# Optimization experiments

Measured on AMD Instinct MI355X. Metric: run time of the kernel, lower is better.

## Reference

```python
import jax, jax.numpy as jnp
import numpy as np

N = 32768   # total nodes
B = 128     # graphs
S = 256     # nodes per graph (equal-size graphs)
E = 524288  # edges
DIN = 128   # in_dim
DH = 256    # hidden_dim
H = 8       # heads
DFF = 1024  # ffn hidden
EPS = 1e-5


def _seg_sum(x, idx, num):
    return jax.ops.segment_sum(x, idx, num_segments=num)


def _bn(x, g, b):
    # BatchNorm1d with batch statistics (training-mode math, deterministic)
    mu = jnp.mean(x, axis=0)
    var = jnp.mean((x - mu) ** 2, axis=0)
    return (x - mu) * jax.lax.rsqrt(var + EPS) * g + b


def _ln(x, g, b):
    mu = jnp.mean(x, axis=-1, keepdims=True)
    var = jnp.mean((x - mu) ** 2, axis=-1, keepdims=True)
    return (x - mu) * jax.lax.rsqrt(var + EPS) * g + b


def _gcn_conv(x, W, bias, edge_index, n):
    # PyG GCNConv: h = x W; add self-loops; norm = d^-1/2[row] * d^-1/2[col]; scatter-add at col
    h = x @ W
    loop = jnp.arange(n)
    row = jnp.concatenate([edge_index[0], loop])
    col = jnp.concatenate([edge_index[1], loop])
    deg = _seg_sum(jnp.ones_like(col, dtype=h.dtype), col, n)  # >=1 due to self-loops
    dis = jax.lax.rsqrt(jnp.maximum(deg, 1.0))
    norm = dis[row] * dis[col]
    out = _seg_sum(h[row] * norm[:, None], col, n)
    return out + bias


def setup_inputs() -> dict:
    key = jax.random.key(0)
    ks = jax.random.split(key, 24)

    def w(i, shape, scale=0.05):
        return jax.random.normal(ks[i], shape, dtype=jnp.float32) * scale

    return {
        "x": jax.random.normal(ks[0], (N, DIN), dtype=jnp.float32),
        "edge_index": jax.random.randint(ks[1], (2, E), 0, N, dtype=jnp.int32),
        "batch": jnp.repeat(jnp.arange(B, dtype=jnp.int32), S),
        "inter_f": jax.random.normal(ks[2], (B, DH), dtype=jnp.float32),
        "bn1_g": jnp.ones((DIN,), jnp.float32), "bn1_b": jnp.zeros((DIN,), jnp.float32),
        "bn2_g": jnp.ones((DH,), jnp.float32), "bn2_b": jnp.zeros((DH,), jnp.float32),
        "w_conv1": w(3, (DIN, DH)), "b_conv1": jnp.zeros((DH,), jnp.float32),
        "w_conv2": w(4, (DH, DH)), "b_conv2": jnp.zeros((DH,), jnp.float32),
        "wq": w(5, (DH, DH)), "bq": jnp.zeros((DH,), jnp.float32),
        "wk": w(6, (DH, DH)), "bk": jnp.zeros((DH,), jnp.float32),
        "wv": w(7, (DH, DH)), "bv": jnp.zeros((DH,), jnp.float32),
        "wo": w(8, (DH, DH)), "bo": jnp.zeros((DH,), jnp.float32),
        "ln1_g": jnp.ones((DH,), jnp.float32), "ln1_b": jnp.zeros((DH,), jnp.float32),
        "ln2_g": jnp.ones((DH,), jnp.float32), "ln2_b": jnp.zeros((DH,), jnp.float32),
        "w_ff1": w(9, (DH, DFF)), "b_ff1": jnp.zeros((DFF,), jnp.float32),
        "w_ff2": w(10, (DFF, DH)), "b_ff2": jnp.zeros((DH,), jnp.float32),
    }


def reference(x, edge_index, batch, inter_f,
              bn1_g, bn1_b, bn2_g, bn2_b,
              w_conv1, b_conv1, w_conv2, b_conv2,
              wq, bq, wk, bk, wv, bv, wo, bo,
              ln1_g, ln1_b, ln2_g, ln2_b,
              w_ff1, b_ff1, w_ff2, b_ff2):
    n = x.shape[0]
    hd = DH // H
    # init_avg_h: scatter-mean of raw x per graph
    cnt = _seg_sum(jnp.ones((n,), x.dtype), batch, B)
    init_avg_h = _seg_sum(x, batch, B) / jnp.maximum(cnt, 1.0)[:, None]
    # layer 1 (dropout = identity in eval)
    h = _bn(x, bn1_g, bn1_b)
    h = jax.nn.relu(_gcn_conv(h, w_conv1, b_conv1, edge_index, n))
    # layer 2 with residual
    pre = h
    h2 = _bn(h, bn2_g, bn2_b)
    h = pre + jax.nn.relu(_gcn_conv(h2, w_conv2, b_conv2, edge_index, n))
    # transformer block: inject per-graph feature, self-attend within each graph
    inter_h = inter_f[batch]
    t = (h + inter_h).reshape(B, S, DH)
    q = (t @ wq + bq).reshape(B, S, H, hd)
    k = (t @ wk + bk).reshape(B, S, H, hd)
    v = (t @ wv + bv).reshape(B, S, H, hd)
    scores = jnp.einsum('bqhd,bkhd->bhqk', q, k) / jnp.sqrt(jnp.float32(hd))
    attn = jax.nn.softmax(scores, axis=-1)
    o = jnp.einsum('bhqk,bkhd->bqhd', attn, v).reshape(B, S, DH) @ wo + bo
    t2 = _ln(t + o, ln1_g, ln1_b)
    ffn = jax.nn.relu(t2 @ w_ff1 + b_ff1) @ w_ff2 + b_ff2
    t3 = _ln(t2 + ffn, ln2_g, ln2_b)
    hg = t3.reshape(n, DH)
    readout = _seg_sum(hg, batch, B)
    return readout, init_avg_h
```

## Files before the change

### kernel.cpp

```cpp
#include <hip/hip_runtime.h>
#include <math.h>

#define NN   32768
#define BG   128
#define SG   256
#define EE   524288
#define DIN_ 128
#define DH_  256
#define NH   8
#define HD_  32
#define DFF_ 1024
#define EPS_ 1e-5f

typedef __attribute__((ext_vector_type(8))) short bf16x8;
typedef __attribute__((ext_vector_type(4))) float f32x4;
typedef __attribute__((ext_vector_type(2))) unsigned int u32x2;
typedef __attribute__((ext_vector_type(4))) unsigned int u32x4;

__device__ __forceinline__ unsigned short f2bf(float f) {
    unsigned int u = __builtin_bit_cast(unsigned int, f);
    unsigned int r = u + 0x7FFFu + ((u >> 16) & 1u);
    return (unsigned short)(r >> 16);
}
__device__ __forceinline__ float bf2f(unsigned short u) {
    return __builtin_bit_cast(float, (unsigned int)u << 16);
}
__device__ __forceinline__ unsigned int pack2bf(float a, float b) {
    return (unsigned int)f2bf(a) | ((unsigned int)f2bf(b) << 16);
}
__device__ __forceinline__ void glds16(const unsigned short* g, unsigned short* l) {
    __builtin_amdgcn_global_load_lds(
        (const __attribute__((address_space(1))) void*)g,
        (__attribute__((address_space(3))) void*)l, 16, 0, 0);
}
#define WAIT_VM4() __builtin_amdgcn_s_waitcnt(0x0F74)
#define WAIT_VM2() __builtin_amdgcn_s_waitcnt(0x0F72)
#define WAIT_VM1() __builtin_amdgcn_s_waitcnt(0x0F71)
#define WAIT_VM0() __builtin_amdgcn_s_waitcnt(0x0F70)

#define QSCALE (0.17677669529663689f * 1.4426950408889634f)

__global__ __launch_bounds__(128) void initavg_kernel(const float* __restrict__ X,
                                                      float* __restrict__ out2) {
    int b = blockIdx.x, j = threadIdx.x;
    float s = 0.f;
    for (int r = 0; r < SG; ++r) s += X[(size_t)(b * SG + r) * DIN_ + j];
    out2[b * DIN_ + j] = s * (1.f / (float)SG);
}

template <int C>
__global__ __launch_bounds__(C) void colstats_kernel(const float* __restrict__ X,
                                                     float* __restrict__ csum,
                                                     float* __restrict__ csumsq) {
    int j = threadIdx.x;
    size_t r0 = (size_t)blockIdx.x * 256;
    float s = 0.f, sq = 0.f;
    for (int r = 0; r < 256; ++r) {
        float v = X[(r0 + r) * C + j];
        s += v; sq += v * v;
    }
    atomicAdd(&csum[j], s);
    atomicAdd(&csumsq[j], sq);
}

template <int C>
__global__ __launch_bounds__(C) void colstats_b_kernel(const unsigned short* __restrict__ X,
                                                       float* __restrict__ csum,
                                                       float* __restrict__ csumsq) {
    int j = threadIdx.x;
    size_t r0 = (size_t)blockIdx.x * 256;
    float s = 0.f, sq = 0.f;
    for (int r = 0; r < 256; ++r) {
        float v = bf2f(X[(r0 + r) * C + j]);
        s += v; sq += v * v;
    }
    atomicAdd(&csum[j], s);
    atomicAdd(&csumsq[j], sq);
}

template <int C>
__global__ __launch_bounds__(C) void bnfin_kernel(const float* __restrict__ csum,
                                                  const float* __restrict__ csumsq,
                                                  const float* __restrict__ g,
                                                  const float* __restrict__ b,
                                                  float* __restrict__ scale,
                                                  float* __restrict__ shift) {
    int j = threadIdx.x;
    float mu  = csum[j] * (1.f / (float)NN);
    float var = csumsq[j] * (1.f / (float)NN) - mu * mu;
    float s = g[j] * rsqrtf(var + EPS_);
    scale[j] = s;
    shift[j] = b[j] - mu * s;
}

template <int C>
__global__ __launch_bounds__(256) void bnapply_kernel(const float* __restrict__ X,
                                                      const float* __restrict__ sc,
                                                      const float* __restrict__ sh,
                                                      unsigned short* __restrict__ Y) {
    int i = blockIdx.x * 256 + threadIdx.x;
    int j = i & (C - 1);
    Y[i] = f2bf(X[i] * sc[j] + sh[j]);
}

__global__ __launch_bounds__(256) void wtrans_kernel(const float* __restrict__ W,
                                                     unsigned short* __restrict__ Wt,
                                                     int K, int N, float scale) {
    int idx = blockIdx.x * 256 + threadIdx.x;
    if (idx < K * N) {
        int n = idx / K, k = idx - n * K;
        Wt[idx] = f2bf(W[(size_t)k * N + n] * scale);
    }
}

__global__ __launch_bounds__(256) void bcat_kernel(const float* __restrict__ bq,
                                                   const float* __restrict__ bk,
                                                   const float* __restrict__ bv,
                                                   float* __restrict__ o) {
    int j = threadIdx.x;
    if (blockIdx.x == 0) o[j] = bq[j] * QSCALE;
    else if (blockIdx.x == 1) o[DH_ + j] = bk[j];
    else o[2 * DH_ + j] = bv[j];
}

__global__ __launch_bounds__(256) void deg_kernel(const int* __restrict__ col,
                                                  int* __restrict__ deg) {
    int e = blockIdx.x * 256 + threadIdx.x;
    if (e < EE) atomicAdd(&deg[col[e]], 1);
}

__global__ __launch_bounds__(1024) void scan_kernel(const int* __restrict__ deg,
                                                    int* __restrict__ off,
                                                    float* __restrict__ dis) {
    __shared__ int sums[1024];
    int t = threadIdx.x;
    int base = t * 32;
    int loc[32];
    int run = 0;
#pragma unroll
    for (int i = 0; i < 32; ++i) { loc[i] = run; run += deg[base + i]; }
    sums[t] = run;
    __syncthreads();
    for (int d = 1; d < 1024; d <<= 1) {
        int tmp = (t >= d) ? sums[t - d] : 0;
        __syncthreads();
        sums[t] += tmp;
        __syncthreads();
    }
    int excl = sums[t] - run;
#pragma unroll
    for (int i = 0; i < 32; ++i) {
        off[base + i] = excl + loc[i];
        dis[base + i] = rsqrtf((float)(deg[base + i] + 1));
    }
    if (t == 1023) off[NN] = sums[1023];
}

__global__ __launch_bounds__(256) void scatter_kernel(const int* __restrict__ row,
                                                      const int* __restrict__ col,
                                                      const int* __restrict__ off,
                                                      int* __restrict__ cnt,
                                                      int* __restrict__ srow) {
    int e = blockIdx.x * 256 + threadIdx.x;
    if (e < EE) {
        int c = col[e];
        int p = off[c] + atomicAdd(&cnt[c], 1);
        srow[p] = row[e];
    }
}

template <int C, int FUSE_BN>
__global__ __launch_bounds__(256) void aggb_kernel(const unsigned short* __restrict__ X,
                                                   const int* __restrict__ off,
                                                   const int* __restrict__ srow,
                                                   const float* __restrict__ dis,
                                                   const float* __restrict__ scl,
                                                   const float* __restrict__ shf,
                                                   unsigned short* __restrict__ Y) {
    constexpr int EPL = C / 64;
    int lane = threadIdx.x & 63;
    int c = blockIdx.x * 4 + (threadIdx.x >> 6);
    float dc = dis[c];
    float acc[EPL];
    float wsum = dc;
    {
        unsigned short t[EPL];
        const unsigned short* xc = X + (size_t)c * C + lane * EPL;
        if constexpr (EPL == 4) *(uint2*)t = *(const uint2*)xc;
        else *(unsigned int*)t = *(const unsigned int*)xc;
#pragma unroll
        for (int e2 = 0; e2 < EPL; ++e2) acc[e2] = dc * bf2f(t[e2]);
    }
    int s = off[c], en = off[c + 1];
    int i = s;
    for (; i + 4 <= en; i += 4) {
        int r0 = srow[i], r1 = srow[i + 1], r2 = srow[i + 2], r3 = srow[i + 3];
        float d0 = dis[r0], d1 = dis[r1], d2 = dis[r2], d3 = dis[r3];
        unsigned short t0[EPL], t1[EPL], t2[EPL], t3[EPL];
        const unsigned short* p0 = X + (size_t)r0 * C + lane * EPL;
        const unsigned short* p1 = X + (size_t)r1 * C + lane * EPL;
        const unsigned short* p2 = X + (size_t)r2 * C + lane * EPL;
        const unsigned short* p3 = X + (size_t)r3 * C + lane * EPL;
        if constexpr (EPL == 4) {
            *(uint2*)t0 = *(const uint2*)p0;
            *(uint2*)t1 = *(const uint2*)p1;
            *(uint2*)t2 = *(const uint2*)p2;
            *(uint2*)t3 = *(const uint2*)p3;
        } else {
            *(unsigned int*)t0 = *(const unsigned int*)p0;
            *(unsigned int*)t1 = *(const unsigned int*)p1;
            *(unsigned int*)t2 = *(const unsigned int*)p2;
            *(unsigned int*)t3 = *(const unsigned int*)p3;
        }
        wsum += d0 + d1 + d2 + d3;
#pragma unroll
        for (int e2 = 0; e2 < EPL; ++e2) {
            acc[e2] += d0 * bf2f(t0[e2]) + d1 * bf2f(t1[e2]) +
                       d2 * bf2f(t2[e2]) + d3 * bf2f(t3[e2]);
        }
    }
    for (; i < en; ++i) {
        int r = srow[i];
        float dr = dis[r];
        unsigned short t[EPL];
        const unsigned short* xr = X + (size_t)r * C + lane * EPL;
        if constexpr (EPL == 4) *(uint2*)t = *(const uint2*)xr;
        else *(unsigned int*)t = *(const unsigned int*)xr;
        wsum += dr;
#pragma unroll
        for (int e2 = 0; e2 < EPL; ++e2) acc[e2] += dr * bf2f(t[e2]);
    }
    unsigned short t[EPL];
#pragma unroll
    for (int e2 = 0; e2 < EPL; ++e2) {
        float v;
        if constexpr (FUSE_BN) {
            int j = lane * EPL + e2;
            v = dc * (scl[j] * acc[e2] + shf[j] * wsum);
        } else {
            v = dc * acc[e2];
        }
        t[e2] = f2bf(v);
    }
    unsigned short* yc = Y + (size_t)c * C + lane * EPL;
    if constexpr (EPL == 4) *(uint2*)yc = *(const uint2*)t;
    else *(unsigned int*)yc = *(const unsigned int*)t;
}

template <int MT>
__global__ __launch_bounds__(512, 8) void gemm_bf16_kernel(
    const unsigned short* __restrict__ A,
    const unsigned short* __restrict__ Bt,
    unsigned short* __restrict__ Cb,
    int M, int K, int N,
    const float* __restrict__ bias,
    const unsigned short* __restrict__ resb,
    const float* __restrict__ inter,
    int do_relu, int relu_first) {
    constexpr int LDP = 32;
    constexpr int CP = 136;
    constexpr int MI = MT / 64;
    constexpr int STG = (MT == 128) ? 8192 : 6144;
    constexpr int BOFS = (MT == 128) ? 4096 : 2048;
    constexpr int SMEMSZ = 3 * STG;
    __shared__ unsigned short Smem[SMEMSZ];
    unsigned short* Cs = Smem;
    int gx = gridDim.x, gyP = gridDim.y >> 3;
    int d = blockIdx.y * gx + blockIdx.x;
    int xcd = d & 7, j2 = d >> 3;
    int bm = (xcd * gyP + j2 / gx) * MT;
    int bn = (j2 % gx) * 128;
    int tid = threadIdx.x;
    int wave = tid >> 6, lane = tid & 63;
    int wm = (wave >> 1) * (MT / 4);
    int wn = (wave & 1) * 64;
    int lrc = lane & 15;
    int koct = lane >> 4;
    int rsw = (lrc >> 1) & 3;
    int rofs = (koct ^ rsw) * 8;

    int cg = (lane & 3) ^ ((lane >> 3) & 3);
    int skk = cg * 8;

    const unsigned short* g0 = nullptr;
    int lofs64 = 0;
    int nloads = 2;
    size_t gstride16 = 0;
    if constexpr (MT == 64) {
        if (wave < 4) {
            int sr = wave * 32 + (lane >> 2);
            g0 = Bt + (size_t)(bn + sr) * K + skk;
            lofs64 = BOFS + wave * 1024 + lane * 8;
            nloads = 2;
            gstride16 = (size_t)16 * K;
        } else {
            int sr = (wave - 4) * 16 + (lane >> 2);
            g0 = A + (size_t)(bm + sr) * K + skk;
            lofs64 = (wave - 4) * 512 + lane * 8;
            nloads = 1;
        }
    }
    const unsigned short* gA0 = nullptr;
    const unsigned short* gB0 = nullptr;
    int lofs = 0;
    if constexpr (MT == 128) {
        int sr = wave * 16 + (lane >> 2);
        gA0 = A + (size_t)(bm + sr) * K + skk;
        gB0 = Bt + (size_t)(bn + sr) * K + skk;
        lofs = wave * 512 + lane * 8;
    }

    f32x4 acc[MI][4];
#pragma unroll
    for (int i = 0; i < MI; ++i)
#pragma unroll
        for (int j = 0; j < 4; ++j) acc[i][j] = (f32x4){0.f, 0.f, 0.f, 0.f};

    if constexpr (MT == 128) {
        glds16(gA0, Smem + lofs);
        glds16(gB0, Smem + BOFS + lofs);
        glds16(gA0 + 32, Smem + STG + lofs);
        glds16(gB0 + 32, Smem + STG + BOFS + lofs);
    } else {
        glds16(g0, Smem + lofs64);
        if (nloads == 2) glds16(g0 + gstride16, Smem + lofs64 + 512);
        glds16(g0 + 32, Smem + STG + lofs64);
        if (nloads == 2) glds16(g0 + 32 + gstride16, Smem + STG + lofs64 + 512);
    }

    int rb = 0;
    for (int k0 = 0; k0 < K; k0 += 32) {
        if (k0 + 64 < K) {
            int wb = rb + 2; if (wb >= 3) wb -= 3;
            unsigned short* ld = Smem + wb * STG;
            if constexpr (MT == 128) {
                glds16(gA0 + k0 + 64, ld + lofs);
                glds16(gB0 + k0 + 64, ld + BOFS + lofs);
                WAIT_VM4();
            } else {
                glds16(g0 + k0 + 64, ld + lofs64);
                if (nloads == 2) {
                    glds16(g0 + k0 + 64 + gstride16, ld + lofs64 + 512);
                    WAIT_VM4();
                } else {
                    WAIT_VM2();
                }
            }
        } else if (k0 + 32 < K) {
            if constexpr (MT == 128) WAIT_VM2();
            else { if (nloads == 2) WAIT_VM2(); else WAIT_VM1(); }
        } else {
            WAIT_VM0();
        }
        __builtin_amdgcn_s_barrier();
        const unsigned short* Ab = Smem + rb * STG;
        const unsigned short* Bb = Ab + BOFS;
        bf16x8 af[MI], bfr[4];
#pragma unroll
        for (int i = 0; i < MI; ++i)
            af[i] = *(const bf16x8*)(Ab + (wm + i * 16 + lrc) * LDP + rofs);
#pragma unroll
        for (int j = 0; j < 4; ++j)
            bfr[j] = *(const bf16x8*)(Bb + (wn + j * 16 + lrc) * LDP + rofs);
#pragma unroll
        for (int i = 0; i < MI; ++i)
#pragma unroll
            for (int j = 0; j < 4; ++j)
                acc[i][j] = __builtin_amdgcn_mfma_f32_16x16x32_bf16(af[i], bfr[j],
                                                                    acc[i][j], 0, 0, 0);
        __builtin_amdgcn_s_barrier();
        rb = (rb + 1 == 3) ? 0 : rb + 1;
    }
#pragma unroll
    for (int i = 0; i < MI; ++i) {
#pragma unroll
        for (int r = 0; r < 4; ++r) {
            int lrow = wm + i * 16 + koct * 4 + r;
            int grow = bm + lrow;
#pragma unroll
            for (int j = 0; j < 4; ++j) {
                int lcol = wn + j * 16 + lrc;
                int gcol = bn + lcol;
                float v = acc[i][j][r];
                if (bias) v += bias[gcol];
                if (relu_first) v = fmaxf(v, 0.f);
                if (resb) v += bf2f(resb[(size_t)grow * N + gcol]);
                if (inter) v += inter[(grow >> 8) * N + gcol];
                if (do_relu && !relu_first) v = fmaxf(v, 0.f);
                Cs[lrow * CP + lcol] = f2bf(v);
            }
        }
    }
    __syncthreads();
#pragma unroll
    for (int it = 0; it < MT / 32; ++it) {
        int row = it * 32 + (tid >> 4);
        int cc = (tid & 15) * 8;
        *(uint4*)(&Cb[(size_t)(bm + row) * N + bn + cc]) =
            *(const uint4*)(&Cs[row * CP + cc]);
    }
}

__global__ __launch_bounds__(256, 4) void attn_mfma_kernel(
    const unsigned short* __restrict__ QKV,
    unsigned short* __restrict__ Ob) {
    int b = blockIdx.x >> 3, h = blockIdx.x & 7;
    __shared__ unsigned short Ks[256 * 32];
    __shared__ unsigned short Vt[32 * 264];
    __shared__ float Lc[4 * 64];
    const unsigned short* kg = QKV + (size_t)b * 256 * 768 + 256 + h * 32;
    const unsigned short* vg = QKV + (size_t)b * 256 * 768 + 512 + h * 32;
    int tid = threadIdx.x;
#pragma unroll
    for (int it = 0; it < 4; ++it) {
        int c = it * 256 + tid;
        int row = c >> 2, ch = c & 3;
        int slot = ch ^ ((row >> 1) & 3);
        *(uint4*)(Ks + row * 32 + slot * 8) =
            *(const uint4*)(kg + (size_t)row * 768 + ch * 8);
    }
#pragma unroll
    for (int it = 0; it < 4; ++it) {
        int c = it * 256 + tid;
        int key = c >> 2, d0 = (c & 3) * 8;
        unsigned short tmp[8];
        *(uint4*)tmp = *(const uint4*)(vg + (size_t)key * 768 + d0);
#pragma unroll
        for (int j = 0; j < 8; ++j) Vt[(d0 + j) * 264 + key] = tmp[j];
    }
    __syncthreads();

    int wave = tid >> 6, lane = tid & 63;
    int lr = lane & 15, koct = lane >> 4;
    int s4 = (lr >> 1) & 3;
    int qrow0 = b * 256 + wave * 64;
    bf16x8 qf[4];
#pragma unroll
    for (int j = 0; j < 4; ++j)
        qf[j] = *(const bf16x8*)(QKV + (size_t)(qrow0 + j * 16 + lr) * 768 + h * 32 + koct * 8);

    f32x4 Oa[4][2];
    float lp[4];
#pragma unroll
    for (int i = 0; i < 4; ++i) {
        Oa[i][0] = (f32x4){0.f, 0.f, 0.f, 0.f};
        Oa[i][1] = (f32x4){0.f, 0.f, 0.f, 0.f};
        lp[i] = 0.f;
    }
    float* Lw = Lc + wave * 64;

    for (int kc = 0; kc < 256; kc += 32) {
        bf16x8 kf0 = *(const bf16x8*)(Ks + (kc + lr) * 32 + (koct ^ s4) * 8);
        bf16x8 kf1 = *(const bf16x8*)(Ks + (kc + 16 + lr) * 32 + (koct ^ s4) * 8);
        bf16x8 pfr[4];
#pragma unroll
        for (int j = 0; j < 4; ++j) {
            f32x4 St0 = __builtin_amdgcn_mfma_f32_16x16x32_bf16(kf0, qf[j],
                            (f32x4){0.f, 0.f, 0.f, 0.f}, 0, 0, 0);
            f32x4 St1 = __builtin_amdgcn_mfma_f32_16x16x32_bf16(kf1, qf[j],
                            (f32x4){0.f, 0.f, 0.f, 0.f}, 0, 0, 0);
            float p0[4], p1[4], ps = 0.f;
#pragma unroll
            for (int r = 0; r < 4; ++r) {
                p0[r] = exp2f(St0[r]); p1[r] = exp2f(St1[r]);
                ps += p0[r] + p1[r];
            }
            lp[j] += ps;
            unsigned int w0a, w0b, w1a, w1b;
            asm("v_cvt_pk_bf16_f32 %0, %1, %2" : "=v"(w0a) : "v"(p0[0]), "v"(p0[1]));
            asm("v_cvt_pk_bf16_f32 %0, %1, %2" : "=v"(w0b) : "v"(p0[2]), "v"(p0[3]));
            asm("v_cvt_pk_bf16_f32 %0, %1, %2" : "=v"(w1a) : "v"(p1[0]), "v"(p1[1]));
            asm("v_cvt_pk_bf16_f32 %0, %1, %2" : "=v"(w1b) : "v"(p1[2]), "v"(p1[3]));
            u32x2 sa = __builtin_amdgcn_permlane32_swap(w0a, w1a, false, false);
            u32x2 da = __builtin_amdgcn_permlane16_swap(sa[0], sa[1], false, false);
            u32x2 sb = __builtin_amdgcn_permlane32_swap(w0b, w1b, false, false);
            u32x2 db = __builtin_amdgcn_permlane16_swap(sb[0], sb[1], false, false);
            u32x4 pw = {da[0], db[0], da[1], db[1]};
            pfr[j] = __builtin_bit_cast(bf16x8, pw);
        }
        bf16x8 vf0 = *(const bf16x8*)(Vt + lr * 264 + kc + koct * 8);
        bf16x8 vf1 = *(const bf16x8*)(Vt + (16 + lr) * 264 + kc + koct * 8);
#pragma unroll
        for (int i = 0; i < 4; ++i) {
            Oa[i][0] = __builtin_amdgcn_mfma_f32_16x16x32_bf16(pfr[i], vf0, Oa[i][0], 0, 0, 0);
            Oa[i][1] = __builtin_amdgcn_mfma_f32_16x16x32_bf16(pfr[i], vf1, Oa[i][1], 0, 0, 0);
        }
    }
#pragma unroll
    for (int j = 0; j < 4; ++j) {
        lp[j] += __shfl_xor(lp[j], 16);
        lp[j] += __shfl_xor(lp[j], 32);
    }
    if (koct == 0) {
#pragma unroll
        for (int j = 0; j < 4; ++j) Lw[j * 16 + lr] = lp[j];
    }
    __builtin_amdgcn_s_waitcnt(0);
#pragma unroll
    for (int i = 0; i < 4; ++i) {
        f32x4 l4 = *(const f32x4*)(Lw + i * 16 + koct * 4);
#pragma unroll
        for (int r = 0; r < 4; ++r) {
            float inv = 1.f / l4[r];
            int row = qrow0 + i * 16 + koct * 4 + r;
#pragma unroll
            for (int jn = 0; jn < 2; ++jn) {
                int col = h * 32 + jn * 16 + lr;
                Ob[(size_t)row * 256 + col] = f2bf(Oa[i][jn][r] * inv);
            }
        }
    }
}

__global__ __launch_bounds__(256) void lnb_kernel(const unsigned short* __restrict__ Z,
                                                  unsigned short* __restrict__ Out,
                                                  const float* __restrict__ g,
                                                  const float* __restrict__ bt) {
    int row = blockIdx.x * 4 + (threadIdx.x >> 6);
    int lane = threadIdx.x & 63;
    unsigned short tv[4];
    *(uint2*)tv = *(const uint2*)(Z + (size_t)row * DH_ + lane * 4);
    float v[4];
    float sum = 0.f;
#pragma unroll
    for (int i = 0; i < 4; ++i) { v[i] = bf2f(tv[i]); sum += v[i]; }
#pragma unroll
    for (int off = 32; off; off >>= 1) sum += __shfl_xor(sum, off);
    float mu = sum * (1.f / (float)DH_);
    float vs = 0.f;
#pragma unroll
    for (int i = 0; i < 4; ++i) { float dd = v[i] - mu; vs += dd * dd; }
#pragma unroll
    for (int off = 32; off; off >>= 1) vs += __shfl_xor(vs, off);
    float rs = rsqrtf(vs * (1.f / (float)DH_) + EPS_);
    float4 gv = *(const float4*)(g + lane * 4);
    float4 bv = *(const float4*)(bt + lane * 4);
    unsigned short ov[4];
    ov[0] = f2bf((v[0] - mu) * rs * gv.x + bv.x);
    ov[1] = f2bf((v[1] - mu) * rs * gv.y + bv.y);
    ov[2] = f2bf((v[2] - mu) * rs * gv.z + bv.z);
    ov[3] = f2bf((v[3] - mu) * rs * gv.w + bv.w);
    *(uint2*)(Out + (size_t)row * DH_ + lane * 4) = *(uint2*)ov;
}

__global__ __launch_bounds__(256) void readout_kernel(const unsigned short* __restrict__ T3,
                                                      float* __restrict__ out) {
    int b = blockIdx.x, j = threadIdx.x;
    float s = 0.f;
    for (int r = 0; r < SG; ++r) s += bf2f(T3[(size_t)(b * SG + r) * DH_ + j]);
    out[b * DH_ + j] = s;
}

extern "C" void kernel_launch(void* const* d_in, const int* in_sizes, int n_in,
                              void* d_out, int out_size, void* d_ws, size_t ws_size,
                              hipStream_t stream) {
    const float* x       = (const float*)d_in[0];
    const int*   ei      = (const int*)d_in[1];
    const float* inter_f = (const float*)d_in[3];
    const float* bn1_g = (const float*)d_in[4],  *bn1_b = (const float*)d_in[5];
    const float* bn2_g = (const float*)d_in[6],  *bn2_b = (const float*)d_in[7];
    const float* w_conv1 = (const float*)d_in[8],  *b_conv1 = (const float*)d_in[9];
    const float* w_conv2 = (const float*)d_in[10], *b_conv2 = (const float*)d_in[11];
    const float* wq = (const float*)d_in[12], *bq = (const float*)d_in[13];
    const float* wk = (const float*)d_in[14], *bk = (const float*)d_in[15];
    const float* wv = (const float*)d_in[16], *bv = (const float*)d_in[17];
    const float* wo = (const float*)d_in[18], *bo = (const float*)d_in[19];
    const float* ln1_g = (const float*)d_in[20], *ln1_b = (const float*)d_in[21];
    const float* ln2_g = (const float*)d_in[22], *ln2_b = (const float*)d_in[23];
    const float* w_ff1 = (const float*)d_in[24], *b_ff1 = (const float*)d_in[25];
    const float* w_ff2 = (const float*)d_in[26], *b_ff2 = (const float*)d_in[27];
    float* out = (float*)d_out;

    char* base = (char*)d_ws;
    size_t o = 0;
    auto alloc = [&](size_t bytes) -> void* {
        void* p = base + o;
        o = (o + bytes + 255) & ~(size_t)255;
        return p;
    };
    int*   deg    = (int*)alloc(NN * 4);
    int*   off    = (int*)alloc((NN + 1) * 4);
    int*   cnt    = (int*)alloc(NN * 4);
    int*   srow   = (int*)alloc(EE * 4);
    float* dis    = (float*)alloc(NN * 4);
    float* csum   = (float*)alloc(256 * 4);
    float* csumsq = (float*)alloc(256 * 4);
    float* scl    = (float*)alloc(256 * 4);
    float* shf    = (float*)alloc(256 * 4);
    float* bqkv   = (float*)alloc(768 * 4);
    const size_t SLOT = (size_t)NN * DH_;
    unsigned short* Arena = (unsigned short*)alloc((size_t)NN * DFF_ * 2);
    unsigned short* TB = (unsigned short*)alloc(SLOT * 2);
    unsigned short* B0 = (unsigned short*)alloc(SLOT * 2);
    unsigned short* wc1t  = (unsigned short*)alloc((size_t)DIN_ * DH_ * 2);
    unsigned short* wc2t  = (unsigned short*)alloc((size_t)DH_ * DH_ * 2);
    unsigned short* wqkvt = (unsigned short*)alloc((size_t)DH_ * DH_ * 3 * 2);
    unsigned short* wot   = (unsigned short*)alloc((size_t)DH_ * DH_ * 2);
    unsigned short* wf1t  = (unsigned short*)alloc((size_t)DH_ * DFF_ * 2);
    unsigned short* wf2t  = (unsigned short*)alloc((size_t)DFF_ * DH_ * 2);
    unsigned short* Xa   = Arena;
    unsigned short* X2a  = Arena + (size_t)NN * DIN_;
    unsigned short* QKVb = Arena;
    unsigned short* zb   = Arena + SLOT * 3;
    unsigned short* Fb   = Arena;
    unsigned short* tb   = TB;
    unsigned short* z2b  = TB;

    hipMemsetAsync(deg, 0, NN * 4, stream);
    hipMemsetAsync(cnt, 0, NN * 4, stream);
    hipMemsetAsync(csum, 0, 2048, stream);

    wtrans_kernel<<<(DIN_ * DH_ + 255) / 256, 256, 0, stream>>>(w_conv1, wc1t, DIN_, DH_, 1.f);
    wtrans_kernel<<<(DH_ * DH_ + 255) / 256, 256, 0, stream>>>(w_conv2, wc2t, DH_, DH_, 1.f);
    wtrans_kernel<<<(DH_ * DH_ + 255) / 256, 256, 0, stream>>>(wq, wqkvt, DH_, DH_, QSCALE);
    wtrans_kernel<<<(DH_ * DH_ + 255) / 256, 256, 0, stream>>>(wk, wqkvt + DH_ * DH_, DH_, DH_, 1.f);
    wtrans_kernel<<<(DH_ * DH_ + 255) / 256, 256, 0, stream>>>(wv, wqkvt + 2 * DH_ * DH_, DH_, DH_, 1.f);
    wtrans_kernel<<<(DH_ * DH_ + 255) / 256, 256, 0, stream>>>(wo, wot, DH_, DH_, 1.f);
    wtrans_kernel<<<(DH_ * DFF_ + 255) / 256, 256, 0, stream>>>(w_ff1, wf1t, DH_, DFF_, 1.f);
    wtrans_kernel<<<(DFF_ * DH_ + 255) / 256, 256, 0, stream>>>(w_ff2, wf2t, DFF_, DH_, 1.f);
    bcat_kernel<<<3, 256, 0, stream>>>(bq, bk, bv, bqkv);

    initavg_kernel<<<BG, 128, 0, stream>>>(x, out + BG * DH_);

    colstats_kernel<DIN_><<<NN / 256, DIN_, 0, stream>>>(x, csum, csumsq);
    bnfin_kernel<DIN_><<<1, DIN_, 0, stream>>>(csum, csumsq, bn1_g, bn1_b, scl, shf);
    bnapply_kernel<DIN_><<<NN * DIN_ / 256, 256, 0, stream>>>(x, scl, shf, B0);

    deg_kernel<<<EE / 256, 256, 0, stream>>>(ei + EE, deg);
    scan_kernel<<<1, 1024, 0, stream>>>(deg, off, dis);
    scatter_kernel<<<EE / 256, 256, 0, stream>>>(ei, ei + EE, off, cnt, srow);

    aggb_kernel<DIN_, 0><<<NN / 4, 256, 0, stream>>>(B0, off, srow, dis,
                                                     nullptr, nullptr, Xa);
    gemm_bf16_kernel<64><<<dim3(DH_ / 128, NN / 64), 512, 0, stream>>>(
        Xa, wc1t, B0, NN, DIN_, DH_, b_conv1, nullptr, nullptr, 1, 0);

    hipMemsetAsync(csum, 0, 2048, stream);
    colstats_b_kernel<DH_><<<NN / 256, DH_, 0, stream>>>(B0, csum, csumsq);
    bnfin_kernel<DH_><<<1, DH_, 0, stream>>>(csum, csumsq, bn2_g, bn2_b, scl, shf);

    aggb_kernel<DH_, 1><<<NN / 4, 256, 0, stream>>>(B0, off, srow, dis,
                                                    scl, shf, X2a);
    gemm_bf16_kernel<64><<<dim3(DH_ / 128, NN / 64), 512, 0, stream>>>(
        X2a, wc2t, tb, NN, DH_, DH_, b_conv2, B0, inter_f, 1, 1);

    gemm_bf16_kernel<128><<<dim3(768 / 128, NN / 128), 512, 0, stream>>>(
        tb, wqkvt, QKVb, NN, DH_, 768, bqkv, nullptr, nullptr, 0, 0);

    attn_mfma_kernel<<<BG * NH, 256, 0, stream>>>(QKVb, B0);

    gemm_bf16_kernel<64><<<dim3(DH_ / 128, NN / 64), 512, 0, stream>>>(
        B0, wot, zb, NN, DH_, DH_, bo, tb, nullptr, 0, 0);
    lnb_kernel<<<NN / 4, 256, 0, stream>>>(zb, B0, ln1_g, ln1_b);

    gemm_bf16_kernel<128><<<dim3(DFF_ / 128, NN / 128), 512, 0, stream>>>(
        B0, wf1t, Fb, NN, DH_, DFF_, b_ff1, nullptr, nullptr, 1, 0);
    gemm_bf16_kernel<128><<<dim3(DH_ / 128, NN / 128), 512, 0, stream>>>(
        Fb, wf2t, z2b, NN, DFF_, DH_, b_ff2, B0, nullptr, 0, 0);

    lnb_kernel<<<NN / 4, 256, 0, stream>>>(z2b, B0, ln2_g, ln2_b);
    readout_kernel<<<BG, 256, 0, stream>>>(B0, out);
}
```

Measured before the change: 537.4 us.

## Use 4-wave 128x128 GEMM kernel with 64x64 per-wave tiles for QKV and FFN

Adds a dedicated 256-thread GEMM kernel for the 128x128 tile cases, where each wave computes a 64x64 sub-tile (4x4 MFMA fragments) instead of the 8-wave 32x64 layout. Each wave now issues four global-to-LDS loads per stage, with the wait counts adjusted to match. The intent is more register-level reuse of A/B fragments per LDS read and fewer waves per block, lowering LDS traffic and barrier cost. The trade-off is higher register pressure (occupancy bound of 3 blocks per SIMD) and less latency hiding. The generic kernel is simplified to its 64-row path only.

```diff
diff --git a/kernel.cpp b/kernel.cpp
--- a/kernel.cpp
+++ b/kernel.cpp
@@ -33,6 +33,7 @@
         (const __attribute__((address_space(1))) void*)g,
         (__attribute__((address_space(3))) void*)l, 16, 0, 0);
 }
+#define WAIT_VM8() __builtin_amdgcn_s_waitcnt(0x0F78)
 #define WAIT_VM4() __builtin_amdgcn_s_waitcnt(0x0F74)
 #define WAIT_VM2() __builtin_amdgcn_s_waitcnt(0x0F72)
 #define WAIT_VM1() __builtin_amdgcn_s_waitcnt(0x0F71)
@@ -260,8 +261,8 @@
     constexpr int LDP = 32;
     constexpr int CP = 136;
     constexpr int MI = MT / 64;
-    constexpr int STG = (MT == 128) ? 8192 : 6144;
-    constexpr int BOFS = (MT == 128) ? 4096 : 2048;
+    constexpr int STG = 6144;
+    constexpr int BOFS = 2048;
     constexpr int SMEMSZ = 3 * STG;
     __shared__ unsigned short Smem[SMEMSZ];
     unsigned short* Cs = Smem;
@@ -286,28 +287,17 @@
     int lofs64 = 0;
     int nloads = 2;
     size_t gstride16 = 0;
-    if constexpr (MT == 64) {
-        if (wave < 4) {
-            int sr = wave * 32 + (lane >> 2);
-            g0 = Bt + (size_t)(bn + sr) * K + skk;
-            lofs64 = BOFS + wave * 1024 + lane * 8;
-            nloads = 2;
-            gstride16 = (size_t)16 * K;
-        } else {
-            int sr = (wave - 4) * 16 + (lane >> 2);
-            g0 = A + (size_t)(bm + sr) * K + skk;
-            lofs64 = (wave - 4) * 512 + lane * 8;
-            nloads = 1;
-        }
-    }
-    const unsigned short* gA0 = nullptr;
-    const unsigned short* gB0 = nullptr;
-    int lofs = 0;
-    if constexpr (MT == 128) {
-        int sr = wave * 16 + (lane >> 2);
-        gA0 = A + (size_t)(bm + sr) * K + skk;
-        gB0 = Bt + (size_t)(bn + sr) * K + skk;
-        lofs = wave * 512 + lane * 8;
+    if (wave < 4) {
+        int sr = wave * 32 + (lane >> 2);
+        g0 = Bt + (size_t)(bn + sr) * K + skk;
+        lofs64 = BOFS + wave * 1024 + lane * 8;
+        nloads = 2;
+        gstride16 = (size_t)16 * K;
+    } else {
+        int sr = (wave - 4) * 16 + (lane >> 2);
+        g0 = A + (size_t)(bm + sr) * K + skk;
+        lofs64 = (wave - 4) * 512 + lane * 8;
+        nloads = 1;
     }
 
     f32x4 acc[MI][4];
@@ -316,39 +306,25 @@
 #pragma unroll
         for (int j = 0; j < 4; ++j) acc[i][j] = (f32x4){0.f, 0.f, 0.f, 0.f};
 
-    if constexpr (MT == 128) {
-        glds16(gA0, Smem + lofs);
-        glds16(gB0, Smem + BOFS + lofs);
-        glds16(gA0 + 32, Smem + STG + lofs);
-        glds16(gB0 + 32, Smem + STG + BOFS + lofs);
-    } else {
-        glds16(g0, Smem + lofs64);
-        if (nloads == 2) glds16(g0 + gstride16, Smem + lofs64 + 512);
-        glds16(g0 + 32, Smem + STG + lofs64);
-        if (nloads == 2) glds16(g0 + 32 + gstride16, Smem + STG + lofs64 + 512);
-    }
+    glds16(g0, Smem + lofs64);
+    if (nloads == 2) glds16(g0 + gstride16, Smem + lofs64 + 512);
+    glds16(g0 + 32, Smem + STG + lofs64);
+    if (nloads == 2) glds16(g0 + 32 + gstride16, Smem + STG + lofs64 + 512);
 
     int rb = 0;
     for (int k0 = 0; k0 < K; k0 += 32) {
         if (k0 + 64 < K) {
             int wb = rb + 2; if (wb >= 3) wb -= 3;
             unsigned short* ld = Smem + wb * STG;
-            if constexpr (MT == 128) {
-                glds16(gA0 + k0 + 64, ld + lofs);
-                glds16(gB0 + k0 + 64, ld + BOFS + lofs);
+            glds16(g0 + k0 + 64, ld + lofs64);
+            if (nloads == 2) {
+                glds16(g0 + k0 + 64 + gstride16, ld + lofs64 + 512);
                 WAIT_VM4();
             } else {
-                glds16(g0 + k0 + 64, ld + lofs64);
-                if (nloads == 2) {
-                    glds16(g0 + k0 + 64 + gstride16, ld + lofs64 + 512);
-                    WAIT_VM4();
-                } else {
-                    WAIT_VM2();
-                }
+                WAIT_VM2();
             }
         } else if (k0 + 32 < K) {
-            if constexpr (MT == 128) WAIT_VM2();
-            else { if (nloads == 2) WAIT_VM2(); else WAIT_VM1(); }
+            if (nloads == 2) WAIT_VM2(); else WAIT_VM1();
         } else {
             WAIT_VM0();
         }
@@ -395,6 +371,122 @@
 #pragma unroll
     for (int it = 0; it < MT / 32; ++it) {
         int row = it * 32 + (tid >> 4);
+        int cc = (tid & 15) * 8;
+        *(uint4*)(&Cb[(size_t)(bm + row) * N + bn + cc]) =
+            *(const uint4*)(&Cs[row * CP + cc]);
+    }
+}
+
+__global__ __launch_bounds__(256, 3) void gemm128w4_kernel(
+    const unsigned short* __restrict__ A,
+    const unsigned short* __restrict__ Bt,
+    unsigned short* __restrict__ Cb,
+    int M, int K, int N,
+    const float* __restrict__ bias,
+    const unsigned short* __restrict__ resb,
+    const float* __restrict__ inter,
+    int do_relu, int relu_first) {
+    constexpr int LDP = 32;
+    constexpr int CP = 136;
+    constexpr int STG = 8192;
+    constexpr int BOFS = 4096;
+    __shared__ unsigned short Smem[3 * STG];
+    unsigned short* Cs = Smem;
+    int gx = gridDim.x, gyP = gridDim.y >> 3;
+    int d = blockIdx.y * gx + blockIdx.x;
+    int xcd = d & 7, j2 = d >> 3;
+    int bm = (xcd * gyP + j2 / gx) * 128;
+    int bn = (j2 % gx) * 128;
+    int tid = threadIdx.x;
+    int wave = tid >> 6, lane = tid & 63;
+    int wm = (wave >> 1) * 64;
+    int wn = (wave & 1) * 64;
+    int lrc = lane & 15;
+    int koct = lane >> 4;
+    int rsw = (lrc >> 1) & 3;
+    int rofs = (koct ^ rsw) * 8;
+    int cg = (lane & 3) ^ ((lane >> 3) & 3);
+    int skk = cg * 8;
+
+    int sr = wave * 32 + (lane >> 2);
+    const unsigned short* gA0 = A + (size_t)(bm + sr) * K + skk;
+    const unsigned short* gB0 = Bt + (size_t)(bn + sr) * K + skk;
+    size_t g16 = (size_t)16 * K;
+    int lofs = wave * 1024 + lane * 8;
+
+    f32x4 acc[4][4];
+#pragma unroll
+    for (int i = 0; i < 4; ++i)
+#pragma unroll
+        for (int j = 0; j < 4; ++j) acc[i][j] = (f32x4){0.f, 0.f, 0.f, 0.f};
+
+#pragma unroll
+    for (int st = 0; st < 2; ++st) {
+        unsigned short* s = Smem + st * STG;
+        glds16(gA0 + st * 32, s + lofs);
+        glds16(gA0 + st * 32 + g16, s + lofs + 512);
+        glds16(gB0 + st * 32, s + BOFS + lofs);
+        glds16(gB0 + st * 32 + g16, s + BOFS + lofs + 512);
+    }
+
+    int rb = 0;
+    for (int k0 = 0; k0 < K; k0 += 32) {
+        if (k0 + 64 < K) {
+            int wb = rb + 2; if (wb >= 3) wb -= 3;
+            unsigned short* s = Smem + wb * STG;
+            glds16(gA0 + k0 + 64, s + lofs);
+            glds16(gA0 + k0 + 64 + g16, s + lofs + 512);
+            glds16(gB0 + k0 + 64, s + BOFS + lofs);
+            glds16(gB0 + k0 + 64 + g16, s + BOFS + lofs + 512);
+            WAIT_VM8();
+        } else if (k0 + 32 < K) {
+            WAIT_VM4();
+        } else {
+            WAIT_VM0();
+        }
+        __builtin_amdgcn_s_barrier();
+        const unsigned short* Ab = Smem + rb * STG;
+        const unsigned short* Bb = Ab + BOFS;
+        bf16x8 af[4], bfr[4];
+#pragma unroll
+        for (int i = 0; i < 4; ++i)
+            af[i] = *(const bf16x8*)(Ab + (wm + i * 16 + lrc) * LDP + rofs);
+#pragma unroll
+        for (int j = 0; j < 4; ++j)
+            bfr[j] = *(const bf16x8*)(Bb + (wn + j * 16 + lrc) * LDP + rofs);
+#pragma unroll
+        for (int i = 0; i < 4; ++i)
+#pragma unroll
+            for (int j = 0; j < 4; ++j)
+                acc[i][j] = __builtin_amdgcn_mfma_f32_16x16x32_bf16(af[i], bfr[j],
+                                                                    acc[i][j], 0, 0, 0);
+        __builtin_amdgcn_s_barrier();
+        rb = (rb + 1 == 3) ? 0 : rb + 1;
+    }
+#pragma unroll
+    for (int i = 0; i < 4; ++i) {
+#pragma unroll
+        for (int r = 0; r < 4; ++r) {
+            int lrow = wm + i * 16 + koct * 4 + r;
+            int grow = bm + lrow;
+#pragma unroll
+            for (int j = 0; j < 4; ++j) {
+                int lcol = wn + j * 16 + lrc;
+                int gcol = bn + lcol;
+                float v = acc[i][j][r];
+                if (bias) v += bias[gcol];
+                if (relu_first) v = fmaxf(v, 0.f);
+                if (resb) v += bf2f(resb[(size_t)grow * N + gcol]);
+                if (inter) v += inter[(grow >> 8) * N + gcol];
+                if (do_relu && !relu_first) v = fmaxf(v, 0.f);
+                Cs[lrow * CP + lcol] = f2bf(v);
+            }
+        }
+    }
+    __syncthreads();
+#pragma unroll
+    for (int it = 0; it < 8; ++it) {
+        int row = it * 16 + (tid >> 4);
         int cc = (tid & 15) * 8;
         *(uint4*)(&Cb[(size_t)(bm + row) * N + bn + cc]) =
             *(const uint4*)(&Cs[row * CP + cc]);
@@ -644,7 +736,7 @@
     gemm_bf16_kernel<64><<<dim3(DH_ / 128, NN / 64), 512, 0, stream>>>(
         X2a, wc2t, tb, NN, DH_, DH_, b_conv2, B0, inter_f, 1, 1);
 
-    gemm_bf16_kernel<128><<<dim3(768 / 128, NN / 128), 512, 0, stream>>>(
+    gemm128w4_kernel<<<dim3(768 / 128, NN / 128), 256, 0, stream>>>(
         tb, wqkvt, QKVb, NN, DH_, 768, bqkv, nullptr, nullptr, 0, 0);
 
     attn_mfma_kernel<<<BG * NH, 256, 0, stream>>>(QKVb, B0);
@@ -653,9 +745,9 @@
         B0, wot, zb, NN, DH_, DH_, bo, tb, nullptr, 0, 0);
     lnb_kernel<<<NN / 4, 256, 0, stream>>>(zb, B0, ln1_g, ln1_b);
 
-    gemm_bf16_kernel<128><<<dim3(DFF_ / 128, NN / 128), 512, 0, stream>>>(
+    gemm128w4_kernel<<<dim3(DFF_ / 128, NN / 128), 256, 0, stream>>>(
         B0, wf1t, Fb, NN, DH_, DFF_, b_ff1, nullptr, nullptr, 1, 0);
-    gemm_bf16_kernel<128><<<dim3(DH_ / 128, NN / 128), 512, 0, stream>>>(
+    gemm128w4_kernel<<<dim3(DH_ / 128, NN / 128), 256, 0, stream>>>(
         Fb, wf2t, z2b, NN, DFF_, DH_, b_ff2, B0, nullptr, 0, 0);
 
     lnb_kernel<<<NN / 4, 256, 0, stream>>>(z2b, B0, ln2_g, ln2_b);
```

New measurement: 567.3 us. 5.6% more time.
